# Kernel optimization log

Hardware: AMD Instinct MI355X
Metric: run time of the kernel (lower is better)

The kernel has to match this reference:

```python
import jax, jax.numpy as jnp
import numpy as np

B, N, HID, HEADS, LAYERS, POOL = 2, 2048, 256, 4, 2, 128
D = HID // HEADS  # per-head dim


def attn_pool(x, w1, b1, w2, b2):
    # x: [B,N,HID]; mask is all-ones in this module's forward, so plain softmax
    s = jnp.tanh(x @ w1 + b1) @ w2 + b2            # [B,N]
    a = jax.nn.softmax(s, axis=-1)                  # [B,N]
    return jnp.einsum('bn,bnc->bc', a, x)           # [B,HID]


def gat_layer(x, adj_mask, proj_w, a_src, a_dst):
    # x: [B,N,HID] -> h: [B,N,HEADS,D]
    h = (x @ proj_w).reshape(x.shape[0], x.shape[1], HEADS, D)
    src = jnp.einsum('bnhd,hd->bnh', h, a_src)      # [B,N,H]
    dst = jnp.einsum('bnhd,hd->bnh', h, a_dst)      # [B,N,H]
    logits = src[:, :, None, :] + dst[:, None, :, :]  # [B,i,j,H]
    logits = jnp.where(logits >= 0, logits, 0.2 * logits)  # leaky_relu(0.2)
    logits = jnp.where(adj_mask[..., None], logits, jnp.float32(-1e9))
    attn = jax.nn.softmax(logits, axis=2)           # softmax over j (neighbors)
    out = jnp.einsum('bijh,bjhd->bihd', attn, h)
    return out.reshape(x.shape[0], x.shape[1], HEADS * D)


def setup_inputs() -> dict:
    key = jax.random.key(0)
    ks = jax.random.split(key, 16)
    sd = 0.05
    gene_expr = jax.random.normal(ks[0], (B, N), dtype=jnp.float32)
    gene_adj = jax.random.randint(ks[1], (B, N, N), 0, 2, dtype=jnp.int32)
    in_w = jax.random.normal(ks[2], (HID,), dtype=jnp.float32) * sd
    in_b = jax.random.normal(ks[3], (HID,), dtype=jnp.float32) * sd
    proj_w = jax.random.normal(ks[4], (LAYERS, HID, HID), dtype=jnp.float32) * sd
    attn_src = jax.random.normal(ks[5], (LAYERS, HEADS, D), dtype=jnp.float32) * sd
    attn_dst = jax.random.normal(ks[6], (LAYERS, HEADS, D), dtype=jnp.float32) * sd
    pool_w1 = jax.random.normal(ks[7], (LAYERS, HID, POOL), dtype=jnp.float32) * sd
    pool_b1 = jax.random.normal(ks[8], (LAYERS, POOL), dtype=jnp.float32) * sd
    pool_w2 = jax.random.normal(ks[9], (LAYERS, POOL), dtype=jnp.float32) * sd
    pool_b2 = jax.random.normal(ks[10], (LAYERS,), dtype=jnp.float32) * sd
    ip_w1 = jax.random.normal(ks[11], (HID, POOL), dtype=jnp.float32) * sd
    ip_b1 = jax.random.normal(ks[12], (POOL,), dtype=jnp.float32) * sd
    ip_w2 = jax.random.normal(ks[13], (POOL,), dtype=jnp.float32) * sd
    ip_b2 = jax.random.normal(ks[14], (), dtype=jnp.float32) * sd
    return dict(gene_expr=gene_expr, gene_adj=gene_adj, in_w=in_w, in_b=in_b,
                proj_w=proj_w, attn_src=attn_src, attn_dst=attn_dst,
                pool_w1=pool_w1, pool_b1=pool_b1, pool_w2=pool_w2, pool_b2=pool_b2,
                ip_w1=ip_w1, ip_b1=ip_b1, ip_w2=ip_w2, ip_b2=ip_b2)


def reference(gene_expr, gene_adj, in_w, in_b, proj_w, attn_src, attn_dst,
              pool_w1, pool_b1, pool_w2, pool_b2, ip_w1, ip_b1, ip_w2, ip_b2):
    # input_proj: Linear(1, HID) on gene_expr[...,None], then relu
    x = jax.nn.relu(gene_expr[:, :, None] * in_w + in_b)  # [B,N,HID]
    raw_pooled = attn_pool(x, ip_w1, ip_b1, ip_w2, ip_b2)
    adj_mask = gene_adj > 0
    node_outs, pooled_outs = [], []
    cur = x
    for l in range(LAYERS):
        cur = gat_layer(cur, adj_mask, proj_w[l], attn_src[l], attn_dst[l])
        cur = jax.nn.elu(cur)
        node_outs.append(cur)
        pooled_outs.append(attn_pool(cur, pool_w1[l], pool_b1[l], pool_w2[l], pool_b2[l]))
    # (raw_pooled, node_out_0, node_out_1, pooled_0, pooled_1); final_pooled == pooled_outs[-1]
    return (raw_pooled, *node_outs, *pooled_outs)
```

## Files before the change

kernel.cpp:

```cpp
#include <hip/hip_runtime.h>
#include <hip/hip_bf16.h>

#define B_ 2
#define N_ 2048
#define HID_ 256
#define HEADS_ 4
#define D_ 64
#define POOL_ 128

typedef __bf16 bf16;
typedef __bf16 bf16x8 __attribute__((ext_vector_type(8)));
typedef float f32x4 __attribute__((ext_vector_type(4)));

__device__ __forceinline__ float fast_tanh(float x) {
    x = fminf(fmaxf(x, -15.f), 15.f);
    float t = __expf(2.f * x);
    return (t - 1.f) / (t + 1.f);
}

__global__ void k_setup(const int* __restrict__ adj, unsigned* __restrict__ am,
                        const float* __restrict__ ge, const float* __restrict__ iw,
                        const float* __restrict__ ib, bf16* __restrict__ xb,
                        const float* __restrict__ proj_w, const float* __restrict__ ipw1,
                        const float* __restrict__ pw1, bf16* __restrict__ wT0,
                        bf16* __restrict__ wT1, bf16* __restrict__ ipw1T,
                        bf16* __restrict__ w1T0, bf16* __restrict__ w1T1) {
    int blk = blockIdx.x, tid = threadIdx.x;
    if (blk < 32768) {
        int gid = blk * 256 + tid;
        int v = adj[gid];
        unsigned long long mask = __ballot(v > 0);
        int lane = tid & 63;
        if (lane == 0) am[gid >> 5] = (unsigned)mask;
        else if (lane == 32) am[gid >> 5] = (unsigned)(mask >> 32);
    } else if (blk < 36864) {
        int row = blk - 32768;
        float g = ge[row];
        float v = fmaxf(g * iw[tid] + ib[tid], 0.f);
        xb[row * HID_ + tid] = (bf16)v;
    } else {
        int o = (blk - 36864) * 256 + tid;
        const float* src; bf16* dst; int Nc, loc;
        if (o < 65536)       { src = proj_w;         dst = wT0;   Nc = 256; loc = o; }
        else if (o < 131072) { src = proj_w + 65536; dst = wT1;   Nc = 256; loc = o - 65536; }
        else if (o < 163840) { src = ipw1;           dst = ipw1T; Nc = 128; loc = o - 131072; }
        else if (o < 196608) { src = pw1;            dst = w1T0;  Nc = 128; loc = o - 163840; }
        else                 { src = pw1 + 32768;    dst = w1T1;  Nc = 128; loc = o - 196608; }
        int n = loc >> 8, k = loc & 255;
        dst[loc] = (bf16)src[k * Nc + n];
    }
}

__device__ __forceinline__ void pool_sw_body(const bf16* __restrict__ A,
                                             const bf16* __restrict__ W1T,
                                             const float* __restrict__ b1,
                                             const float* __restrict__ w2,
                                             const float* __restrict__ b2,
                                             float* __restrict__ part,
                                             float* __restrict__ pz,
                                             int slot, int b, int ch, char* smemraw) {
    int n0 = ch * 16;
    int tid = threadIdx.x;
    int w = tid >> 6, lane = tid & 63, r = lane & 15, g = lane >> 4;
    const bf16* ap = A + ((long long)(b * N_ + n0) + r) * 256 + g * 8;
    f32x4 acc[2] = {{0,0,0,0},{0,0,0,0}};
    for (int ks = 0; ks < 256; ks += 32) {
        bf16x8 af = *(const bf16x8*)(ap + ks);
        #pragma unroll
        for (int nf = 0; nf < 2; ++nf) {
            bf16x8 bfr = *(const bf16x8*)(W1T + (w * 32 + nf * 16 + r) * 256 + ks + g * 8);
            acc[nf] = __builtin_amdgcn_mfma_f32_16x16x32_bf16(af, bfr, acc[nf], 0, 0, 0);
        }
    }
    float b1v[2], w2v[2];
    #pragma unroll
    for (int nf = 0; nf < 2; ++nf) {
        b1v[nf] = b1[w * 32 + nf * 16 + r];
        w2v[nf] = w2[w * 32 + nf * 16 + r];
    }
    float (*pred)[16] = (float (*)[16])smemraw;
    float* el = (float*)(smemraw + 256);
    #pragma unroll
    for (int q = 0; q < 4; ++q) {
        float p = fast_tanh(acc[0][q] + b1v[0]) * w2v[0] + fast_tanh(acc[1][q] + b1v[1]) * w2v[1];
        p += __shfl_xor(p, 1); p += __shfl_xor(p, 2);
        p += __shfl_xor(p, 4); p += __shfl_xor(p, 8);
        if (r == 0) pred[w][g * 4 + q] = p;
    }
    __syncthreads();
    if (tid < 16) {
        float s = pred[0][tid] + pred[1][tid] + pred[2][tid] + pred[3][tid] + b2[0];
        el[tid] = __expf(s);
    }
    __syncthreads();
    if (tid == 0) {
        float z = 0.f;
        #pragma unroll
        for (int n = 0; n < 16; ++n) z += el[n];
        pz[(slot * B_ + b) * 128 + ch] = z;
    }
    const bf16* xp = A + (long long)(b * N_ + n0) * 256 + tid;
    float accum = 0.f;
    #pragma unroll
    for (int n = 0; n < 16; ++n) accum += el[n] * (float)xp[n * 256];
    part[(((long long)slot * B_ + b) * 128 + ch) * 256 + tid] = accum;
}

__global__ __launch_bounds__(256) void k_gemm_h_pool(const bf16* __restrict__ A,
                                                     const bf16* __restrict__ WT,
                                                     const float* __restrict__ as,
                                                     const float* __restrict__ ad,
                                                     bf16* __restrict__ hbT,
                                                     float* __restrict__ srcM,
                                                     float* __restrict__ dstT,
                                                     const bf16* __restrict__ W1T,
                                                     const float* __restrict__ b1,
                                                     const float* __restrict__ w2,
                                                     const float* __restrict__ b2,
                                                     float* __restrict__ part,
                                                     float* __restrict__ pz, int slot) {
    __shared__ __align__(16) char smem[16640];
    int blk = blockIdx.x;
    if (blk >= 256) {
        int pb = blk - 256;
        pool_sw_body(A, W1T, b1, w2, b2, part, pz, slot, pb >> 7, pb & 127, smem);
        return;
    }
    int i0 = (blk & 63) * 64, hd = blk >> 6;
    int n0 = hd * 64;
    int w = threadIdx.x >> 6, lane = threadIdx.x & 63, r = lane & 15, g = lane >> 4;
    const bf16* ap = A + (i0 + w * 16 + r) * 256 + g * 8;
    f32x4 acc[4] = {{0,0,0,0},{0,0,0,0},{0,0,0,0},{0,0,0,0}};
    for (int ks = 0; ks < 256; ks += 32) {
        bf16x8 af = *(const bf16x8*)(ap + ks);
        #pragma unroll
        for (int nf = 0; nf < 4; ++nf) {
            bf16x8 bfr = *(const bf16x8*)(WT + (n0 + nf * 16 + r) * 256 + ks + g * 8);
            acc[nf] = __builtin_amdgcn_mfma_f32_16x16x32_bf16(af, bfr, acc[nf], 0, 0, 0);
        }
    }
    int b = i0 >> 11, nbase = i0 & 2047;
    int bh = b * HEADS_ + hd;
    float asv[4], adv[4];
    #pragma unroll
    for (int nf = 0; nf < 4; ++nf) {
        asv[nf] = as[hd * 64 + nf * 16 + r];
        adv[nf] = ad[hd * 64 + nf * 16 + r];
    }
    float (*tr)[65] = (float (*)[65])smem;
    #pragma unroll
    for (int q = 0; q < 4; ++q) {
        int ln = w * 16 + g * 4 + q;
        float ps = 0.f, pd = 0.f;
        #pragma unroll
        for (int nf = 0; nf < 4; ++nf) {
            float v = acc[nf][q];
            ps += v * asv[nf];
            pd += v * adv[nf];
            tr[nf * 16 + r][ln] = v;
        }
        ps += __shfl_xor(ps, 1); ps += __shfl_xor(ps, 2);
        ps += __shfl_xor(ps, 4); ps += __shfl_xor(ps, 8);
        pd += __shfl_xor(pd, 1); pd += __shfl_xor(pd, 2);
        pd += __shfl_xor(pd, 4); pd += __shfl_xor(pd, 8);
        if (r == 0) {
            srcM[bh * N_ + nbase + ln] = ps;
            dstT[bh * N_ + nbase + ln] = pd;
        }
    }
    __syncthreads();
    int ld = threadIdx.x >> 2, ln0 = (threadIdx.x & 3) * 16;
    bf16x8 o0, o1;
    #pragma unroll
    for (int e = 0; e < 8; ++e) {
        o0[e] = (bf16)tr[ld][ln0 + e];
        o1[e] = (bf16)tr[ld][ln0 + 8 + e];
    }
    bf16* hp = hbT + ((long long)bh * D_ + ld) * N_ + nbase + ln0;
    *(bf16x8*)(hp) = o0;
    *(bf16x8*)(hp + 8) = o1;
}

__global__ __launch_bounds__(256) void k_pool_sw(const bf16* __restrict__ A,
                                                 const bf16* __restrict__ W1T,
                                                 const float* __restrict__ b1,
                                                 const float* __restrict__ w2,
                                                 const float* __restrict__ b2,
                                                 float* __restrict__ part,
                                                 float* __restrict__ pz, int slot) {
    __shared__ __align__(16) char smem[320];
    pool_sw_body(A, W1T, b1, w2, b2, part, pz, slot, blockIdx.y, blockIdx.x, smem);
}

__global__ __launch_bounds__(512, 4) void k_attn(const float* __restrict__ srcM,
                                                 const float* __restrict__ dstT,
                                                 const unsigned* __restrict__ am,
                                                 const bf16* __restrict__ hbT,
                                                 float* __restrict__ nodeOut,
                                                 bf16* __restrict__ xbNext) {
    int it = blockIdx.x, hd = blockIdx.y, b = blockIdx.z;
    int i0 = it * 32;
    int tid = threadIdx.x;
    int w = tid >> 6, lane = tid & 63, r = lane & 15, g = lane >> 4;
    int rg = w >> 2, wj = w & 3;
    int bh = b * HEADS_ + hd;
    const float* drow = dstT + bh * N_;
    const bf16* vbase = hbT + (long long)bh * D_ * N_;

    __shared__ __align__(16) char smem[34816];
    bf16* vt = (bf16*)smem;
    float (*accs)[16][68] = (float (*)[16][68])smem;
    __shared__ float lred[8][16];

    int i = i0 + rg * 16 + r;
    const unsigned* mrow = am + ((long long)(b * N_ + i)) * 64;
    float sv = srcM[bh * N_ + i];

    f32x4 acc[4] = {{0,0,0,0},{0,0,0,0},{0,0,0,0},{0,0,0,0}};
    float l = 0.f;

    bf16x8 st[4];
    #pragma unroll
    for (int k = 0; k < 4; ++k) {
        int s = tid + k * 512, d = s >> 5, seg = s & 31;
        st[k] = *(const bf16x8*)(vbase + d * N_ + seg * 8);
    }

    #pragma unroll
    for (int t = 0; t < 8; ++t) {
        #pragma unroll
        for (int k = 0; k < 4; ++k) {
            int s = tid + k * 512, d = s >> 5, seg = s & 31;
            *(bf16x8*)(vt + d * 264 + seg * 8) = st[k];
        }
        __syncthreads();
        if (t < 7) {
            #pragma unroll
            for (int k = 0; k < 4; ++k) {
                int s = tid + k * 512, d = s >> 5, seg = s & 31;
                st[k] = *(const bf16x8*)(vbase + d * N_ + (t + 1) * 256 + seg * 8);
            }
        }
        #pragma unroll
        for (int s = 0; s < 2; ++s) {
            int jb = t * 256 + wj * 64 + s * 32 + g * 8;
            float4 dv0 = *(const float4*)(drow + jb);
            float4 dv1 = *(const float4*)(drow + jb + 4);
            unsigned mb = (mrow[t * 8 + wj * 2 + s] >> (g * 8)) & 0xFFu;
            float dd[8] = {dv0.x, dv0.y, dv0.z, dv0.w, dv1.x, dv1.y, dv1.z, dv1.w};
            bf16x8 af;
            float es[8];
            #pragma unroll
            for (int tt = 0; tt < 8; ++tt) {
                float s2 = sv + dd[tt];
                float lv = fmaxf(s2, 0.2f * s2);
                float e2 = __expf(lv);
                e2 = ((mb >> tt) & 1u) ? e2 : 0.f;
                es[tt] = e2;
                af[tt] = (bf16)e2;
            }
            l += ((es[0] + es[1]) + (es[2] + es[3])) + ((es[4] + es[5]) + (es[6] + es[7]));
            #pragma unroll
            for (int nf = 0; nf < 4; ++nf) {
                bf16x8 vf = *(const bf16x8*)(vt + (nf * 16 + r) * 264 + wj * 64 + s * 32 + g * 8);
                acc[nf] = __builtin_amdgcn_mfma_f32_16x16x32_bf16(af, vf, acc[nf], 0, 0, 0);
            }
        }
        __syncthreads();
    }

    l += __shfl_xor(l, 16);
    l += __shfl_xor(l, 32);
    if (g == 0) lred[w][r] = l;
    #pragma unroll
    for (int nf = 0; nf < 4; ++nf)
        #pragma unroll
        for (int q = 0; q < 4; ++q)
            accs[w][g * 4 + q][nf * 16 + r] = acc[nf][q];
    __syncthreads();

    int cc = lane;
    #pragma unroll
    for (int k = 0; k < 4; ++k) {
        int rr = w * 4 + k;
        int rg2 = rr >> 4, rl = rr & 15;
        float ls = 0.f, v = 0.f;
        #pragma unroll
        for (int w2 = 0; w2 < 4; ++w2) {
            ls += lred[rg2 * 4 + w2][rl];
            v += accs[rg2 * 4 + w2][rl][cc];
        }
        v /= ls;
        float o = v > 0.f ? v : expm1f(v);
        int idx = (b * N_ + i0 + rr) * HID_ + hd * D_ + cc;
        nodeOut[idx] = o;
        xbNext[idx] = (bf16)o;
    }
}

__global__ __launch_bounds__(256) void k_pool_finals(const float* __restrict__ part,
                                                     const float* __restrict__ pz,
                                                     float* __restrict__ outRaw,
                                                     float* __restrict__ pool0,
                                                     float* __restrict__ pool1) {
    int slot = blockIdx.x >> 1, b = blockIdx.x & 1;
    int tid = threadIdx.x;
    int lane = tid & 63, w = tid >> 6;
    float z = (tid < 128) ? pz[(slot * B_ + b) * 128 + tid] : 0.f;
    #pragma unroll
    for (int o = 1; o < 64; o <<= 1) z += __shfl_xor(z, o);
    __shared__ float red[4];
    if (lane == 0) red[w] = z;
    __syncthreads();
    float Z = red[0] + red[1] + red[2] + red[3];
    float acc = 0.f;
    #pragma unroll 8
    for (int ch = 0; ch < 128; ++ch)
        acc += part[(((long long)slot * B_ + b) * 128 + ch) * 256 + tid];
    float* out = slot == 0 ? outRaw : (slot == 1 ? pool0 : pool1);
    out[b * HID_ + tid] = acc / Z;
}

extern "C" void kernel_launch(void* const* d_in, const int* in_sizes, int n_in,
                              void* d_out, int out_size, void* d_ws, size_t ws_size,
                              hipStream_t stream) {
    const float* ge     = (const float*)d_in[0];
    const int*   adj    = (const int*)d_in[1];
    const float* in_w   = (const float*)d_in[2];
    const float* in_b   = (const float*)d_in[3];
    const float* proj_w = (const float*)d_in[4];
    const float* a_src  = (const float*)d_in[5];
    const float* a_dst  = (const float*)d_in[6];
    const float* pw1    = (const float*)d_in[7];
    const float* pb1    = (const float*)d_in[8];
    const float* pw2    = (const float*)d_in[9];
    const float* pb2    = (const float*)d_in[10];
    const float* ipw1   = (const float*)d_in[11];
    const float* ipb1   = (const float*)d_in[12];
    const float* ipw2   = (const float*)d_in[13];
    const float* ipb2   = (const float*)d_in[14];

    char* ws = (char*)d_ws;
    bf16*     xb    = (bf16*)(ws + 0);
    bf16*     hbT   = (bf16*)(ws + 2097152);
    float*    srcM  = (float*)(ws + 4194304);
    float*    dstT  = (float*)(ws + 4259840);
    unsigned* am    = (unsigned*)(ws + 4325376);
    bf16*     wT0   = (bf16*)(ws + 5373952);
    bf16*     wT1   = wT0 + 65536;
    bf16*     ipw1T = wT1 + 65536;
    bf16*     w1T0  = ipw1T + 32768;
    bf16*     w1T1  = w1T0 + 32768;
    float*    part  = (float*)(ws + 5832704);
    float*    pz    = (float*)(ws + 6619136);

    float* outRaw = (float*)d_out;
    float* node0  = outRaw + 512;
    float* node1  = node0 + 1048576;
    float* pool0  = node1 + 1048576;
    float* pool1  = pool0 + 512;

    k_setup<<<37760, 256, 0, stream>>>(adj, am, ge, in_w, in_b, xb,
                                       proj_w, ipw1, pw1, wT0, wT1, ipw1T, w1T0, w1T1);

    k_gemm_h_pool<<<512, 256, 0, stream>>>(xb, wT0, a_src, a_dst, hbT, srcM, dstT,
                                           ipw1T, ipb1, ipw2, ipb2, part, pz, 0);
    k_attn<<<dim3(64, 4, 2), 512, 0, stream>>>(srcM, dstT, am, hbT, node0, xb);

    k_gemm_h_pool<<<512, 256, 0, stream>>>(xb, wT1, a_src + 256, a_dst + 256, hbT, srcM, dstT,
                                           w1T0, pb1, pw2, pb2, part, pz, 1);
    k_attn<<<dim3(64, 4, 2), 512, 0, stream>>>(srcM, dstT, am, hbT, node1, xb);

    k_pool_sw<<<dim3(128, B_), 256, 0, stream>>>(xb, w1T1, pb1 + POOL_, pw2 + 1, pb2 + 1,
                                                 part, pz, 2);
    k_pool_finals<<<6, 256, 0, stream>>>(part, pz, outRaw, pool0, pool1);
}
```

Baseline: 105.1 us.

## Fuse pool finalization via last-block atomics, stage GEMM in LDS, double-buffer attention V

Removes the separate pool-finals kernel: each pooling block increments an atomic counter, and the last block for a (slot, batch) pair reduces the partials and writes the pooled output. The projection GEMM now stages its A and W tiles in padded LDS before the MFMA loop instead of reading fragments straight from global memory. The attention kernel double-buffers the V tiles in LDS, prefetching two tiles ahead, which drops one barrier per iteration. Shared memory per block grows to 66 KB in both the GEMM and attention kernels, which may lower occupancy.

```diff
diff --git a/kernel.cpp b/kernel.cpp
--- a/kernel.cpp
+++ b/kernel.cpp
@@ -24,7 +24,8 @@
                         const float* __restrict__ proj_w, const float* __restrict__ ipw1,
                         const float* __restrict__ pw1, bf16* __restrict__ wT0,
                         bf16* __restrict__ wT1, bf16* __restrict__ ipw1T,
-                        bf16* __restrict__ w1T0, bf16* __restrict__ w1T1) {
+                        bf16* __restrict__ w1T0, bf16* __restrict__ w1T1,
+                        int* __restrict__ pcnt) {
     int blk = blockIdx.x, tid = threadIdx.x;
     if (blk < 32768) {
         int gid = blk * 256 + tid;
@@ -39,6 +40,7 @@
         float v = fmaxf(g * iw[tid] + ib[tid], 0.f);
         xb[row * HID_ + tid] = (bf16)v;
     } else {
+        if (blk == 36864 && tid < 8) pcnt[tid] = 0;
         int o = (blk - 36864) * 256 + tid;
         const float* src; bf16* dst; int Nc, loc;
         if (o < 65536)       { src = proj_w;         dst = wT0;   Nc = 256; loc = o; }
@@ -58,7 +60,11 @@
                                              const float* __restrict__ b2,
                                              float* __restrict__ part,
                                              float* __restrict__ pz,
-                                             int slot, int b, int ch, char* smemraw) {
+                                             int slot, int b, int ch, char* smemraw,
+                                             float* __restrict__ outRaw,
+                                             float* __restrict__ pool0,
+                                             float* __restrict__ pool1,
+                                             int* __restrict__ pcnt) {
     int n0 = ch * 16;
     int tid = threadIdx.x;
     int w = tid >> 6, lane = tid & 63, r = lane & 15, g = lane >> 4;
@@ -80,6 +86,8 @@
     }
     float (*pred)[16] = (float (*)[16])smemraw;
     float* el = (float*)(smemraw + 256);
+    int* isLast = (int*)(smemraw + 320);
+    float* red = (float*)(smemraw + 336);
     #pragma unroll
     for (int q = 0; q < 4; ++q) {
         float p = fast_tanh(acc[0][q] + b1v[0]) * w2v[0] + fast_tanh(acc[1][q] + b1v[1]) * w2v[1];
@@ -104,6 +112,28 @@
     #pragma unroll
     for (int n = 0; n < 16; ++n) accum += el[n] * (float)xp[n * 256];
     part[(((long long)slot * B_ + b) * 128 + ch) * 256 + tid] = accum;
+
+    __threadfence();
+    if (tid == 0) {
+        int done = atomicAdd(&pcnt[slot * 2 + b], 1);
+        *isLast = (done == 127) ? 1 : 0;
+    }
+    __syncthreads();
+    if (*isLast) {
+        __threadfence();
+        float z = (tid < 128) ? pz[(slot * B_ + b) * 128 + tid] : 0.f;
+        #pragma unroll
+        for (int o = 1; o < 64; o <<= 1) z += __shfl_xor(z, o);
+        if (lane == 0) red[w] = z;
+        __syncthreads();
+        float Z = red[0] + red[1] + red[2] + red[3];
+        float facc = 0.f;
+        #pragma unroll 8
+        for (int c2 = 0; c2 < 128; ++c2)
+            facc += part[(((long long)slot * B_ + b) * 128 + c2) * 256 + tid];
+        float* out = slot == 0 ? outRaw : (slot == 1 ? pool0 : pool1);
+        out[b * HID_ + tid] = facc / Z;
+    }
 }
 
 __global__ __launch_bounds__(256) void k_gemm_h_pool(const bf16* __restrict__ A,
@@ -118,27 +148,42 @@
                                                      const float* __restrict__ w2,
                                                      const float* __restrict__ b2,
                                                      float* __restrict__ part,
-                                                     float* __restrict__ pz, int slot) {
-    __shared__ __align__(16) char smem[16640];
+                                                     float* __restrict__ pz, int slot,
+                                                     float* __restrict__ outRaw,
+                                                     float* __restrict__ pool0,
+                                                     float* __restrict__ pool1,
+                                                     int* __restrict__ pcnt) {
+    __shared__ __align__(16) char smem[67584];
     int blk = blockIdx.x;
+    int tid = threadIdx.x;
     if (blk >= 256) {
         int pb = blk - 256;
-        pool_sw_body(A, W1T, b1, w2, b2, part, pz, slot, pb >> 7, pb & 127, smem);
+        pool_sw_body(A, W1T, b1, w2, b2, part, pz, slot, pb >> 7, pb & 127, smem,
+                     outRaw, pool0, pool1, pcnt);
         return;
     }
     int i0 = (blk & 63) * 64, hd = blk >> 6;
     int n0 = hd * 64;
-    int w = threadIdx.x >> 6, lane = threadIdx.x & 63, r = lane & 15, g = lane >> 4;
-    const bf16* ap = A + (i0 + w * 16 + r) * 256 + g * 8;
+    int w = tid >> 6, lane = tid & 63, r = lane & 15, g = lane >> 4;
+    bf16* al = (bf16*)smem;
+    bf16* wl = (bf16*)(smem + 33792);
+    #pragma unroll
+    for (int k = 0; k < 8; ++k) {
+        int s = tid + k * 256, d = s >> 5, seg = s & 31;
+        *(bf16x8*)(al + d * 264 + seg * 8) = *(const bf16x8*)(A + (i0 + d) * 256 + seg * 8);
+        *(bf16x8*)(wl + d * 264 + seg * 8) = *(const bf16x8*)(WT + (n0 + d) * 256 + seg * 8);
+    }
+    __syncthreads();
     f32x4 acc[4] = {{0,0,0,0},{0,0,0,0},{0,0,0,0},{0,0,0,0}};
     for (int ks = 0; ks < 256; ks += 32) {
-        bf16x8 af = *(const bf16x8*)(ap + ks);
+        bf16x8 af = *(const bf16x8*)(al + (w * 16 + r) * 264 + ks + g * 8);
         #pragma unroll
         for (int nf = 0; nf < 4; ++nf) {
-            bf16x8 bfr = *(const bf16x8*)(WT + (n0 + nf * 16 + r) * 256 + ks + g * 8);
+            bf16x8 bfr = *(const bf16x8*)(wl + (nf * 16 + r) * 264 + ks + g * 8);
             acc[nf] = __builtin_amdgcn_mfma_f32_16x16x32_bf16(af, bfr, acc[nf], 0, 0, 0);
         }
     }
+    __syncthreads();
     int b = i0 >> 11, nbase = i0 & 2047;
     int bh = b * HEADS_ + hd;
     float asv[4], adv[4];
@@ -169,7 +214,7 @@
         }
     }
     __syncthreads();
-    int ld = threadIdx.x >> 2, ln0 = (threadIdx.x & 3) * 16;
+    int ld = tid >> 2, ln0 = (tid & 3) * 16;
     bf16x8 o0, o1;
     #pragma unroll
     for (int e = 0; e < 8; ++e) {
@@ -187,9 +232,14 @@
                                                  const float* __restrict__ w2,
                                                  const float* __restrict__ b2,
                                                  float* __restrict__ part,
-                                                 float* __restrict__ pz, int slot) {
-    __shared__ __align__(16) char smem[320];
-    pool_sw_body(A, W1T, b1, w2, b2, part, pz, slot, blockIdx.y, blockIdx.x, smem);
+                                                 float* __restrict__ pz, int slot,
+                                                 float* __restrict__ outRaw,
+                                                 float* __restrict__ pool0,
+                                                 float* __restrict__ pool1,
+                                                 int* __restrict__ pcnt) {
+    __shared__ __align__(16) char smem[512];
+    pool_sw_body(A, W1T, b1, w2, b2, part, pz, slot, blockIdx.y, blockIdx.x, smem,
+                 outRaw, pool0, pool1, pcnt);
 }
 
 __global__ __launch_bounds__(512, 4) void k_attn(const float* __restrict__ srcM,
@@ -207,8 +257,7 @@
     const float* drow = dstT + bh * N_;
     const bf16* vbase = hbT + (long long)bh * D_ * N_;
 
-    __shared__ __align__(16) char smem[34816];
-    bf16* vt = (bf16*)smem;
+    __shared__ __align__(16) char smem[67584];
     float (*accs)[16][68] = (float (*)[16][68])smem;
     __shared__ float lred[8][16];
 
@@ -225,35 +274,49 @@
         int s = tid + k * 512, d = s >> 5, seg = s & 31;
         st[k] = *(const bf16x8*)(vbase + d * N_ + seg * 8);
     }
+    #pragma unroll
+    for (int k = 0; k < 4; ++k) {
+        int s = tid + k * 512, d = s >> 5, seg = s & 31;
+        *(bf16x8*)((bf16*)smem + d * 264 + seg * 8) = st[k];
+    }
+    #pragma unroll
+    for (int k = 0; k < 4; ++k) {
+        int s = tid + k * 512, d = s >> 5, seg = s & 31;
+        st[k] = *(const bf16x8*)(vbase + d * N_ + 256 + seg * 8);
+    }
+    __syncthreads();
 
     #pragma unroll
     for (int t = 0; t < 8; ++t) {
-        #pragma unroll
-        for (int k = 0; k < 4; ++k) {
-            int s = tid + k * 512, d = s >> 5, seg = s & 31;
-            *(bf16x8*)(vt + d * 264 + seg * 8) = st[k];
-        }
-        __syncthreads();
+        bf16* bufc = (bf16*)smem + (t & 1) * 16896;
+        bf16* bufn = (bf16*)smem + ((t + 1) & 1) * 16896;
         if (t < 7) {
             #pragma unroll
             for (int k = 0; k < 4; ++k) {
                 int s = tid + k * 512, d = s >> 5, seg = s & 31;
-                st[k] = *(const bf16x8*)(vbase + d * N_ + (t + 1) * 256 + seg * 8);
+                *(bf16x8*)(bufn + d * 264 + seg * 8) = st[k];
             }
         }
-        #pragma unroll
-        for (int s = 0; s < 2; ++s) {
-            int jb = t * 256 + wj * 64 + s * 32 + g * 8;
+        if (t < 6) {
+            #pragma unroll
+            for (int k = 0; k < 4; ++k) {
+                int s = tid + k * 512, d = s >> 5, seg = s & 31;
+                st[k] = *(const bf16x8*)(vbase + d * N_ + (t + 2) * 256 + seg * 8);
+            }
+        }
+        #pragma unroll
+        for (int s2 = 0; s2 < 2; ++s2) {
+            int jb = t * 256 + wj * 64 + s2 * 32 + g * 8;
             float4 dv0 = *(const float4*)(drow + jb);
             float4 dv1 = *(const float4*)(drow + jb + 4);
-            unsigned mb = (mrow[t * 8 + wj * 2 + s] >> (g * 8)) & 0xFFu;
+            unsigned mb = (mrow[t * 8 + wj * 2 + s2] >> (g * 8)) & 0xFFu;
             float dd[8] = {dv0.x, dv0.y, dv0.z, dv0.w, dv1.x, dv1.y, dv1.z, dv1.w};
             bf16x8 af;
             float es[8];
             #pragma unroll
             for (int tt = 0; tt < 8; ++tt) {
-                float s2 = sv + dd[tt];
-                float lv = fmaxf(s2, 0.2f * s2);
+                float s3 = sv + dd[tt];
+                float lv = fmaxf(s3, 0.2f * s3);
                 float e2 = __expf(lv);
                 e2 = ((mb >> tt) & 1u) ? e2 : 0.f;
                 es[tt] = e2;
@@ -262,7 +325,7 @@
             l += ((es[0] + es[1]) + (es[2] + es[3])) + ((es[4] + es[5]) + (es[6] + es[7]));
             #pragma unroll
             for (int nf = 0; nf < 4; ++nf) {
-                bf16x8 vf = *(const bf16x8*)(vt + (nf * 16 + r) * 264 + wj * 64 + s * 32 + g * 8);
+                bf16x8 vf = *(const bf16x8*)(bufc + (nf * 16 + r) * 264 + wj * 64 + s2 * 32 + g * 8);
                 acc[nf] = __builtin_amdgcn_mfma_f32_16x16x32_bf16(af, vf, acc[nf], 0, 0, 0);
             }
         }
@@ -296,29 +359,6 @@
         nodeOut[idx] = o;
         xbNext[idx] = (bf16)o;
     }
-}
-
-__global__ __launch_bounds__(256) void k_pool_finals(const float* __restrict__ part,
-                                                     const float* __restrict__ pz,
-                                                     float* __restrict__ outRaw,
-                                                     float* __restrict__ pool0,
-                                                     float* __restrict__ pool1) {
-    int slot = blockIdx.x >> 1, b = blockIdx.x & 1;
-    int tid = threadIdx.x;
-    int lane = tid & 63, w = tid >> 6;
-    float z = (tid < 128) ? pz[(slot * B_ + b) * 128 + tid] : 0.f;
-    #pragma unroll
-    for (int o = 1; o < 64; o <<= 1) z += __shfl_xor(z, o);
-    __shared__ float red[4];
-    if (lane == 0) red[w] = z;
-    __syncthreads();
-    float Z = red[0] + red[1] + red[2] + red[3];
-    float acc = 0.f;
-    #pragma unroll 8
-    for (int ch = 0; ch < 128; ++ch)
-        acc += part[(((long long)slot * B_ + b) * 128 + ch) * 256 + tid];
-    float* out = slot == 0 ? outRaw : (slot == 1 ? pool0 : pool1);
-    out[b * HID_ + tid] = acc / Z;
 }
 
 extern "C" void kernel_launch(void* const* d_in, const int* in_sizes, int n_in,
@@ -353,6 +393,7 @@
     bf16*     w1T1  = w1T0 + 32768;
     float*    part  = (float*)(ws + 5832704);
     float*    pz    = (float*)(ws + 6619136);
+    int*      pcnt  = (int*)(ws + 6622208);
 
     float* outRaw = (float*)d_out;
     float* node0  = outRaw + 512;
@@ -361,17 +402,18 @@
     float* pool1  = pool0 + 512;
 
     k_setup<<<37760, 256, 0, stream>>>(adj, am, ge, in_w, in_b, xb,
-                                       proj_w, ipw1, pw1, wT0, wT1, ipw1T, w1T0, w1T1);
+                                       proj_w, ipw1, pw1, wT0, wT1, ipw1T, w1T0, w1T1, pcnt);
 
     k_gemm_h_pool<<<512, 256, 0, stream>>>(xb, wT0, a_src, a_dst, hbT, srcM, dstT,
-                                           ipw1T, ipb1, ipw2, ipb2, part, pz, 0);
+                                           ipw1T, ipb1, ipw2, ipb2, part, pz, 0,
+                                           outRaw, pool0, pool1, pcnt);
     k_attn<<<dim3(64, 4, 2), 512, 0, stream>>>(srcM, dstT, am, hbT, node0, xb);
 
     k_gemm_h_pool<<<512, 256, 0, stream>>>(xb, wT1, a_src + 256, a_dst + 256, hbT, srcM, dstT,
-                                           w1T0, pb1, pw2, pb2, part, pz, 1);
+                                           w1T0, pb1, pw2, pb2, part, pz, 1,
+                                           outRaw, pool0, pool1, pcnt);
     k_attn<<<dim3(64, 4, 2), 512, 0, stream>>>(srcM, dstT, am, hbT, node1, xb);
 
     k_pool_sw<<<dim3(128, B_), 256, 0, stream>>>(xb, w1T1, pb1 + POOL_, pw2 + 1, pb2 + 1,
-                                                 part, pz, 2);
-    k_pool_finals<<<6, 256, 0, stream>>>(part, pz, outRaw, pool0, pool1);
-}
+                                                 part, pz, 2, outRaw, pool0, pool1, pcnt);
+}
```

Result: slower. 149.0 us (+41.7%).
